# Optimization experiments

Hardware: AMD Instinct MI355X
Metric: run time of the kernel (lower is better)

Reference implementation:

```python
import math
import jax, jax.numpy as jnp
import numpy as np

B, FIN, FOUT, M = 8192, 512, 512, 8
INV_SQRT_2PI = 1.0 / math.sqrt(2.0 * math.pi)
SQRT_HALF = math.sqrt(0.5)


def setup_inputs() -> dict:
    key = jax.random.key(0)
    k = jax.random.split(key, 7)
    x = jax.random.normal(k[0], (B, FIN), dtype=jnp.float32)
    nan_mask = jax.random.uniform(k[1], (B, FIN)) < 0.15
    nan_mask = nan_mask.at[:, 0].set(True)  # every row has >=1 NaN -> GMM path taken, den > 0
    x = jnp.where(nan_mask, jnp.nan, x)
    bound = 1.0 / math.sqrt(FIN)  # torch nn.Linear default init range
    W = jax.random.uniform(k[2], (FOUT, FIN), dtype=jnp.float32, minval=-bound, maxval=bound)
    b = jax.random.uniform(k[3], (FOUT,), dtype=jnp.float32, minval=-bound, maxval=bound)
    mean_p = 0.1 * jax.random.normal(k[4], (M, FIN), dtype=jnp.float32)
    log_std2 = 0.1 * jax.random.normal(k[5], (M, FIN), dtype=jnp.float32)
    log_weights = jax.random.normal(k[6], (M,), dtype=jnp.float32)
    return {"x": x, "W": W, "b": b, "mean_p": mean_p,
            "log_std2": log_std2, "log_weights": log_weights}


def _nr(z):
    # pdf(z) + z * Phi(z), the Gaussian 'nr' function from the paper
    pdf = INV_SQRT_2PI * jnp.exp(-0.5 * z * z)
    return pdf + z * 0.5 * (1.0 + jax.lax.erf(z * SQRT_HALF))


def reference(x, W, b, mean_p, log_std2, log_weights):
    nan = jnp.isnan(x)                         # [B, FIN]
    empty = jnp.any(nan, axis=-1)[:, None]     # [B, 1]
    mask = nan[:, None, :]                     # [B, 1, FIN]
    # impute NaNs with per-mode GMM means
    mean = jnp.where(mask, mean_p, x[:, None, :])                   # [B, M, FIN]
    num = jnp.einsum('bmf,of->bom', mean, W) + b[None, :, None]     # [B, FOUT, M]
    std2 = jnp.where(mask, jnp.exp(log_std2), jnp.float32(0.0))     # [B, M, FIN]
    den = jnp.sqrt(jnp.einsum('bmf,of->bom', std2, W * W))          # [B, FOUT, M]
    nr = den * _nr(num / (den + 1e-9))                              # [B, FOUT, M]
    mixture = nr @ jax.nn.softmax(log_weights)                      # [B, FOUT]
    return jnp.where(empty, mixture, jax.nn.relu(num[..., 0]))
```

## Files before the change

kernel.cpp:

```cpp
#include <hip/hip_runtime.h>
#include <math.h>

typedef __attribute__((ext_vector_type(8))) short short8;
typedef __attribute__((ext_vector_type(8))) _Float16 f16x8;
typedef __attribute__((ext_vector_type(4))) float floatx4;
typedef __attribute__((ext_vector_type(4))) int intx4;
typedef __attribute__((ext_vector_type(16))) int intx16;

#define B_ROWS 8192
#define FIN    512
#define FOUT   512
#define QSN    4096.0f
#define QINVN  0.000244140625f
#define QSD    32768.0f
#define QINVD  0.000030517578125f

#define WSB_SW   0UL
#define WSB_CNT  64UL
#define WSB_BASE 65536UL
#define WSB_XCH  16842752UL
#define WSB_MSK  25231360UL
#define WSB_WH   33619968UL
#define WSB_BCT  34144256UL

__device__ __forceinline__ void gl2lds16(const void* g, void* l) {
    __builtin_amdgcn_global_load_lds((const __attribute__((address_space(1))) void*)g,
                                     (__attribute__((address_space(3))) void*)l,
                                     16, 0, 0);
}

__device__ __forceinline__ float frcp(float x) { float r; asm("v_rcp_f32 %0, %1" : "=v"(r) : "v"(x)); return r; }
__device__ __forceinline__ float frsq(float x) { float r; asm("v_rsq_f32 %0, %1" : "=v"(r) : "v"(x)); return r; }
__device__ __forceinline__ float fexp2(float x){ float r; asm("v_exp_f32 %0, %1" : "=v"(r) : "v"(x)); return r; }

__global__ __launch_bounds__(256) void prep_all(const float* __restrict__ W,
                                                const float* __restrict__ mean_p,
                                                const float* __restrict__ ls2,
                                                const float* __restrict__ x,
                                                const float* __restrict__ lw,
                                                signed char* __restrict__ bct,
                                                _Float16* __restrict__ Wh,
                                                _Float16* __restrict__ xch,
                                                signed char* __restrict__ msk,
                                                int* __restrict__ cnts,
                                                float* __restrict__ wsf) {
    int tid = threadIdx.x, lane = tid & 63, wid = tid >> 6;
    if (blockIdx.x < 2048) {
        int n  = blockIdx.x * 4 + wid;
        int fc = lane << 3;
        int o = n >> 4, t = n & 15;
        const float* wp = W + (size_t)o * FIN + fc;
        float v[8];
        float qs;
        if (t < 8) {
            const float* mp = mean_p + (size_t)t * FIN + fc;
#pragma unroll
            for (int j = 0; j < 8; ++j) v[j] = mp[j] * wp[j];
            qs = QSN;
            if (t == 0) {
                f16x8 wv;
#pragma unroll
                for (int j = 0; j < 8; ++j) wv[j] = (_Float16)wp[j];
                *(f16x8*)(Wh + (size_t)o * FIN + fc) = wv;
            }
        } else {
            const float* lp = ls2 + (size_t)(t - 8) * FIN + fc;
#pragma unroll
            for (int j = 0; j < 8; ++j) v[j] = fexp2(lp[j] * 1.4426950408889634f) * wp[j] * wp[j];
            qs = QSD;
        }
        unsigned long long pack = 0;
#pragma unroll
        for (int j = 0; j < 8; ++j) {
            int q = (int)rintf(v[j] * qs);
            q = q > 127 ? 127 : (q < -127 ? -127 : q);
            pack |= ((unsigned long long)(unsigned char)(signed char)q) << (8 * j);
        }
        *(unsigned long long*)(bct + (size_t)n * FIN + fc) = pack;
    } else {
        int row = (blockIdx.x - 2048) * 4 + wid;
        const float* xr = x + (size_t)row * FIN + lane * 8;
        float4 a = *(const float4*)xr;
        float4 b = *(const float4*)(xr + 4);
        float v[8] = {a.x, a.y, a.z, a.w, b.x, b.y, b.z, b.w};
        f16x8 xo;
        unsigned long long mpack = 0;
        bool anyn = false;
#pragma unroll
        for (int j = 0; j < 8; ++j) {
            bool isn = (v[j] != v[j]);
            anyn |= isn;
            xo[j] = (_Float16)(isn ? 0.f : v[j]);
            mpack |= ((unsigned long long)(isn ? 1u : 0u)) << (8 * j);
        }
        *(f16x8*)(xch + (size_t)row * FIN + lane * 8) = xo;
        *(unsigned long long*)(msk + (size_t)row * FIN + lane * 8) = mpack;
        bool any = __any(anyn);
        if (lane == 0) cnts[row] = any ? 1 : 0;
        if (blockIdx.x == 2048 && tid == 0) {
            float mx = lw[0];
            for (int m = 1; m < 8; ++m) mx = fmaxf(mx, lw[m]);
            float e[8]; float s = 0.f;
            for (int m = 0; m < 8; ++m) { e[m] = expf(lw[m] - mx); s += e[m]; }
            for (int m = 0; m < 8; ++m) wsf[m] = e[m] / s;
        }
    }
}

__global__ __launch_bounds__(256, 2) void gemm_base(const _Float16* __restrict__ xch,
                                                    const _Float16* __restrict__ Wh,
                                                    _Float16* __restrict__ base) {
    __shared__ char lds[73728];
    int tid = threadIdx.x, lane = tid & 63, wid = tid >> 6;
    int wr = wid >> 1, wc = wid & 1;
    int bb0 = blockIdx.y * 128;
    int ob0 = blockIdx.x * 64;

    const char* xB = (const char*)xch;
    const char* wB = (const char*)Wh;

    int rA0 = (wid +  0) * 8 + (lane >> 3);
    int rA1 = (wid +  4) * 8 + (lane >> 3);
    int rA2 = (wid +  8) * 8 + (lane >> 3);
    int rA3 = (wid + 12) * 8 + (lane >> 3);
    const char* gA0 = xB + (size_t)(bb0 + rA0) * 1024 + (((lane & 7) ^ (rA0 & 7)) << 4);
    const char* gA1 = xB + (size_t)(bb0 + rA1) * 1024 + (((lane & 7) ^ (rA1 & 7)) << 4);
    const char* gA2 = xB + (size_t)(bb0 + rA2) * 1024 + (((lane & 7) ^ (rA2 & 7)) << 4);
    const char* gA3 = xB + (size_t)(bb0 + rA3) * 1024 + (((lane & 7) ^ (rA3 & 7)) << 4);
    const char* gB0 = wB + (size_t)(ob0 + rA0) * 1024 + (((lane & 7) ^ (rA0 & 7)) << 4);
    const char* gB1 = wB + (size_t)(ob0 + rA1) * 1024 + (((lane & 7) ^ (rA1 & 7)) << 4);
    const int lA0o = (wid +  0) * 1024, lA1o = (wid +  4) * 1024;
    const int lA2o = (wid +  8) * 1024, lA3o = (wid + 12) * 1024;
    const int lB0o = 16384 + (wid + 0) * 1024, lB1o = 16384 + (wid + 4) * 1024;

    int offA[4], offB[2];
#pragma unroll
    for (int mi = 0; mi < 4; ++mi) {
        int r = wr * 64 + mi * 16 + (lane & 15);
        offA[mi] = r * 128 + ((((lane >> 4) ^ (r & 7))) << 4);
    }
#pragma unroll
    for (int ni = 0; ni < 2; ++ni) {
        int r = wc * 32 + ni * 16 + (lane & 15);
        offB[ni] = 16384 + r * 128 + ((((lane >> 4) ^ (r & 7))) << 4);
    }

    floatx4 acc[4][2];
#pragma unroll
    for (int mi = 0; mi < 4; ++mi)
#pragma unroll
        for (int ni = 0; ni < 2; ++ni) acc[mi][ni] = (floatx4){0.f, 0.f, 0.f, 0.f};

#define STAGEB(T)                                            \
    {                                                        \
        const int bo_ = ((T) % 3) * 24576;                   \
        gl2lds16(gA0 + (T) * 128, lds + bo_ + lA0o);         \
        gl2lds16(gA1 + (T) * 128, lds + bo_ + lA1o);         \
        gl2lds16(gA2 + (T) * 128, lds + bo_ + lA2o);         \
        gl2lds16(gA3 + (T) * 128, lds + bo_ + lA3o);         \
        gl2lds16(gB0 + (T) * 128, lds + bo_ + lB0o);         \
        gl2lds16(gB1 + (T) * 128, lds + bo_ + lB1o);         \
    }

    STAGEB(0); STAGEB(1);

#pragma unroll
    for (int t = 0; t < 8; ++t) {
        if (t < 7) asm volatile("s_waitcnt vmcnt(6)" ::: "memory");
        else       asm volatile("s_waitcnt vmcnt(0)" ::: "memory");
        __builtin_amdgcn_s_barrier();
        asm volatile("" ::: "memory");
        if (t + 2 < 8) STAGEB(t + 2);

        const int bo = (t % 3) * 24576;
#pragma unroll
        for (int kk = 0; kk < 2; ++kk) {
            const int kx = kk << 6;
            f16x8 av[4], bv[2];
#pragma unroll
            for (int mi = 0; mi < 4; ++mi) av[mi] = *(const f16x8*)(lds + bo + (offA[mi] ^ kx));
#pragma unroll
            for (int ni = 0; ni < 2; ++ni) bv[ni] = *(const f16x8*)(lds + bo + (offB[ni] ^ kx));
            __builtin_amdgcn_s_setprio(1);
#pragma unroll
            for (int mi = 0; mi < 4; ++mi)
#pragma unroll
                for (int ni = 0; ni < 2; ++ni)
                    acc[mi][ni] = __builtin_amdgcn_mfma_f32_16x16x32_f16(av[mi], bv[ni], acc[mi][ni], 0, 0, 0);
            __builtin_amdgcn_s_setprio(0);
        }
    }
#undef STAGEB

#pragma unroll
    for (int mi = 0; mi < 4; ++mi)
#pragma unroll
        for (int ni = 0; ni < 2; ++ni)
#pragma unroll
            for (int r = 0; r < 4; ++r) {
                int row = bb0 + wr * 64 + mi * 16 + (lane >> 4) * 4 + r;
                int col = ob0 + wc * 32 + ni * 16 + (lane & 15);
                base[((size_t)row << 9) + col] = (_Float16)acc[mi][ni][r];
            }
}

__global__ __launch_bounds__(256, 2) void gmm_fused(const signed char* __restrict__ msk,
                                                    const signed char* __restrict__ bct,
                                                    const float* __restrict__ wsf,
                                                    const int* __restrict__ cnts,
                                                    const _Float16* __restrict__ baseh,
                                                    const float* __restrict__ bias,
                                                    float* __restrict__ out) {
    __shared__ char lds[73728];

    int tid = threadIdx.x, lane = tid & 63, wid = tid >> 6;
    int wr = wid >> 1, wc = wid & 1;

    int id = blockIdx.x, g = id >> 8, wi = id & 255;
    int my = (g >> 2) * 16 + (wi >> 4);
    int nx = (g & 3) * 16 + (wi & 15);
    int b0 = my * 256, n0 = nx * 128;

    const char* mB = (const char*)msk;
    const char* bB = (const char*)bct;

    int cl = lane & 31, oh = lane >> 5;
    _Float16 base_r[4][2];
    float bias_r[2];
    int cnt_r[4];
#pragma unroll
    for (int ni = 0; ni < 2; ++ni) bias_r[ni] = bias[nx * 8 + wc * 4 + ni * 2 + oh];
#pragma unroll
    for (int mi = 0; mi < 4; ++mi) {
        int b = b0 + wr * 128 + mi * 32 + cl;
        cnt_r[mi] = cnts[b];
#pragma unroll
        for (int ni = 0; ni < 2; ++ni)
            base_r[mi][ni] = baseh[((size_t)b << 9) + nx * 8 + wc * 4 + ni * 2 + oh];
    }

    int rA0 = (wid +  0) * 16 + (lane >> 2);
    int rA1 = (wid +  4) * 16 + (lane >> 2);
    int rA2 = (wid +  8) * 16 + (lane >> 2);
    int rA3 = (wid + 12) * 16 + (lane >> 2);
    const char* gA0 = mB + (size_t)(b0 + rA0) * 512 + (((lane & 3) ^ ((rA0 >> 1) & 3)) << 4);
    const char* gA1 = mB + (size_t)(b0 + rA1) * 512 + (((lane & 3) ^ ((rA1 >> 1) & 3)) << 4);
    const char* gA2 = mB + (size_t)(b0 + rA2) * 512 + (((lane & 3) ^ ((rA2 >> 1) & 3)) << 4);
    const char* gA3 = mB + (size_t)(b0 + rA3) * 512 + (((lane & 3) ^ ((rA3 >> 1) & 3)) << 4);
    const char* gB0 = bB + (size_t)(n0 + rA0) * 512 + (((lane & 3) ^ ((rA0 >> 1) & 3)) << 4);
    const char* gB1 = bB + (size_t)(n0 + rA1) * 512 + (((lane & 3) ^ ((rA1 >> 1) & 3)) << 4);
    const int lA0o = (wid +  0) * 1024, lA1o = (wid +  4) * 1024;
    const int lA2o = (wid +  8) * 1024, lA3o = (wid + 12) * 1024;
    const int lB0o = 16384 + (wid + 0) * 1024, lB1o = 16384 + (wid + 4) * 1024;

    int offA[4], offB[2];
#pragma unroll
    for (int mi = 0; mi < 4; ++mi) {
        int r = wr * 128 + mi * 32 + (lane & 31);
        offA[mi] = r * 64 + ((((lane >> 5) ^ ((r >> 1) & 3))) << 4);
    }
#pragma unroll
    for (int ni = 0; ni < 2; ++ni) {
        int r = wc * 64 + ni * 32 + (lane & 31);
        offB[ni] = 16384 + r * 64 + ((((lane >> 5) ^ ((r >> 1) & 3))) << 4);
    }

    intx16 acc[4][2];
#pragma unroll
    for (int mi = 0; mi < 4; ++mi)
#pragma unroll
        for (int ni = 0; ni < 2; ++ni)
#pragma unroll
            for (int e = 0; e < 16; ++e) acc[mi][ni][e] = 0;

#define STAGE(T)                                             \
    {                                                        \
        const int bo_ = ((T) % 3) * 24576;                   \
        gl2lds16(gA0 + (T) * 64, lds + bo_ + lA0o);          \
        gl2lds16(gA1 + (T) * 64, lds + bo_ + lA1o);          \
        gl2lds16(gA2 + (T) * 64, lds + bo_ + lA2o);          \
        gl2lds16(gA3 + (T) * 64, lds + bo_ + lA3o);          \
        gl2lds16(gB0 + (T) * 64, lds + bo_ + lB0o);          \
        gl2lds16(gB1 + (T) * 64, lds + bo_ + lB1o);          \
    }

    STAGE(0); STAGE(1);

#pragma unroll
    for (int t = 0; t < 8; ++t) {
        if (t < 7) asm volatile("s_waitcnt vmcnt(6)" ::: "memory");
        else       asm volatile("s_waitcnt vmcnt(0)" ::: "memory");
        __builtin_amdgcn_s_barrier();
        asm volatile("" ::: "memory");
        if (t + 2 < 8) STAGE(t + 2);

        const int bo = (t % 3) * 24576;
#pragma unroll
        for (int kk = 0; kk < 2; ++kk) {
            const int kx = kk << 5;
            intx4 av[4], bv[2];
#pragma unroll
            for (int mi = 0; mi < 4; ++mi) av[mi] = *(const intx4*)(lds + bo + (offA[mi] ^ kx));
#pragma unroll
            for (int ni = 0; ni < 2; ++ni) bv[ni] = *(const intx4*)(lds + bo + (offB[ni] ^ kx));
            __builtin_amdgcn_s_setprio(1);
#pragma unroll
            for (int mi = 0; mi < 4; ++mi)
#pragma unroll
                for (int ni = 0; ni < 2; ++ni)
                    acc[mi][ni] = __builtin_amdgcn_mfma_i32_32x32x32_i8(av[mi], bv[ni], acc[mi][ni], 0, 0, 0);
            __builtin_amdgcn_s_setprio(0);
        }
    }
#undef STAGE

    __syncthreads();

    float swv[8];
#pragma unroll
    for (int m = 0; m < 8; ++m) swv[m] = wsf[m];

    int* sci = (int*)lds + wid * 1056;

#pragma unroll
    for (int mi = 0; mi < 4; ++mi) {
#pragma unroll
        for (int ni = 0; ni < 2; ++ni) {
#pragma unroll
            for (int reg = 0; reg < 16; ++reg) {
                int r = (reg & 3) + 8 * (reg >> 2) + 4 * oh;
                sci[r * 33 + cl] = acc[mi][ni][reg];
            }
            __asm__ volatile("s_waitcnt lgkmcnt(0)" ::: "memory");

            float cn[8], cd[8];
#pragma unroll
            for (int tt = 0; tt < 8; ++tt) cn[tt] = (float)sci[cl * 33 + oh * 16 + tt] * QINVN;
#pragma unroll
            for (int tt = 0; tt < 8; ++tt) cd[tt] = (float)sci[cl * 33 + oh * 16 + 8 + tt] * QINVD;

            int b = b0 + wr * 128 + mi * 32 + cl;
            int o = nx * 8 + wc * 4 + ni * 2 + oh;
            float K0 = (float)base_r[mi][ni] + bias_r[ni];
            bool empty = cnt_r[mi] > 0;

            float mix = 0.f, num0 = 0.f;
#pragma unroll
            for (int m = 0; m < 8; ++m) {
                float num = K0 + cn[m];
                if (m == 0) num0 = num;
                float rs  = frsq(fmaxf(cd[m], 1e-20f));
                float den = cd[m] * rs;
                float z   = num * rs;
                float az  = fabsf(z);
                float E   = fexp2((z * z) * -0.72134752044448170f);
                float t1  = frcp(fmaf(0.2316419f, az, 1.0f));
                float h   = fmaf(t1, 0.5307027145f, -0.7265760135f);
                h = fmaf(t1, h, 0.7107068705f);
                h = fmaf(t1, h, -0.142248368f);
                h = fmaf(t1, h, 0.127414796f);
                float u   = t1 * h;
                float v   = fmaf(-az, u, 0.3989422804014327f);
                float gg  = fmaf(E, v, fmaxf(z, 0.f));
                mix = fmaf(swv[m], den * gg, mix);
            }
            out[((size_t)b << 9) + o] = empty ? mix : fmaxf(num0, 0.f);
        }
    }
}

extern "C" void kernel_launch(void* const* d_in, const int* in_sizes, int n_in,
                              void* d_out, int out_size, void* d_ws, size_t ws_size,
                              hipStream_t stream) {
    const float* x        = (const float*)d_in[0];
    const float* W        = (const float*)d_in[1];
    const float* bvec     = (const float*)d_in[2];
    const float* mean_p   = (const float*)d_in[3];
    const float* log_std2 = (const float*)d_in[4];
    const float* lw       = (const float*)d_in[5];
    float* out = (float*)d_out;

    char* wsb = (char*)d_ws;
    float*        wsf  = (float*)wsb;
    int*          cnts = (int*)(wsb + WSB_CNT);
    _Float16*     base = (_Float16*)(wsb + WSB_BASE);
    _Float16*     xch  = (_Float16*)(wsb + WSB_XCH);
    signed char*  msk  = (signed char*)(wsb + WSB_MSK);
    _Float16*     Wh   = (_Float16*)(wsb + WSB_WH);
    signed char*  bct  = (signed char*)(wsb + WSB_BCT);

    prep_all<<<4096, 256, 0, stream>>>(W, mean_p, log_std2, x, lw, bct, Wh, xch, msk, cnts, wsf);
    gemm_base<<<dim3(FOUT / 64, B_ROWS / 128), 256, 0, stream>>>(xch, Wh, base);
    gmm_fused<<<(B_ROWS / 256) * (8192 / 128), 256, 0, stream>>>(msk, bct, wsf, cnts, base, bvec, out);
}
```

Baseline: 83.57 us.

## Use 8-wave blocks with smaller per-wave tiles and XCD-aware block mapping

The gmm_fused kernel now runs 512 threads per block. Each wave computes a 64x64 output tile instead of 128x64, so the int8 MFMA accumulators and A-fragment loads are halved, and staging is split across 8 waves with fewer async loads per wave. Block-to-tile mapping is also reorganised so consecutive block IDs on the same XCD share row tiles, which should improve L2 reuse. The launch bound asks for 4 blocks of 512 threads, which may cap VGPRs tightly enough to cause spills, and LDS use per block likely still limits residency anyway.

```diff
diff --git a/kernel.cpp b/kernel.cpp
--- a/kernel.cpp
+++ b/kernel.cpp
@@ -204,7 +204,7 @@
             }
 }
 
-__global__ __launch_bounds__(256, 2) void gmm_fused(const signed char* __restrict__ msk,
+__global__ __launch_bounds__(512, 4) void gmm_fused(const signed char* __restrict__ msk,
                                                     const signed char* __restrict__ bct,
                                                     const float* __restrict__ wsf,
                                                     const int* __restrict__ cnts,
@@ -216,47 +216,44 @@
     int tid = threadIdx.x, lane = tid & 63, wid = tid >> 6;
     int wr = wid >> 1, wc = wid & 1;
 
-    int id = blockIdx.x, g = id >> 8, wi = id & 255;
-    int my = (g >> 2) * 16 + (wi >> 4);
-    int nx = (g & 3) * 16 + (wi & 15);
+    int id = blockIdx.x;
+    int xcd = id & 7, pos = id >> 3;
+    int my = xcd * 4 + (pos & 3);
+    int nx = pos >> 2;
     int b0 = my * 256, n0 = nx * 128;
 
     const char* mB = (const char*)msk;
     const char* bB = (const char*)bct;
 
     int cl = lane & 31, oh = lane >> 5;
-    _Float16 base_r[4][2];
+    _Float16 base_r[2][2];
     float bias_r[2];
-    int cnt_r[4];
-#pragma unroll
-    for (int ni = 0; ni < 2; ++ni) bias_r[ni] = bias[nx * 8 + wc * 4 + ni * 2 + oh];
-#pragma unroll
-    for (int mi = 0; mi < 4; ++mi) {
-        int b = b0 + wr * 128 + mi * 32 + cl;
+    int cnt_r[2];
+#pragma unroll
+    for (int ni = 0; ni < 2; ++ni) bias_r[ni] = bias[(n0 >> 4) + wc * 4 + ni * 2 + oh];
+#pragma unroll
+    for (int mi = 0; mi < 2; ++mi) {
+        int b = b0 + wr * 64 + mi * 32 + cl;
         cnt_r[mi] = cnts[b];
 #pragma unroll
         for (int ni = 0; ni < 2; ++ni)
-            base_r[mi][ni] = baseh[((size_t)b << 9) + nx * 8 + wc * 4 + ni * 2 + oh];
-    }
-
-    int rA0 = (wid +  0) * 16 + (lane >> 2);
-    int rA1 = (wid +  4) * 16 + (lane >> 2);
-    int rA2 = (wid +  8) * 16 + (lane >> 2);
-    int rA3 = (wid + 12) * 16 + (lane >> 2);
+            base_r[mi][ni] = baseh[((size_t)b << 9) + (n0 >> 4) + wc * 4 + ni * 2 + oh];
+    }
+
+    int rA0 = (wid + 0) * 16 + (lane >> 2);
+    int rA1 = (wid + 8) * 16 + (lane >> 2);
+    int rB0 = rA0;
     const char* gA0 = mB + (size_t)(b0 + rA0) * 512 + (((lane & 3) ^ ((rA0 >> 1) & 3)) << 4);
     const char* gA1 = mB + (size_t)(b0 + rA1) * 512 + (((lane & 3) ^ ((rA1 >> 1) & 3)) << 4);
-    const char* gA2 = mB + (size_t)(b0 + rA2) * 512 + (((lane & 3) ^ ((rA2 >> 1) & 3)) << 4);
-    const char* gA3 = mB + (size_t)(b0 + rA3) * 512 + (((lane & 3) ^ ((rA3 >> 1) & 3)) << 4);
-    const char* gB0 = bB + (size_t)(n0 + rA0) * 512 + (((lane & 3) ^ ((rA0 >> 1) & 3)) << 4);
-    const char* gB1 = bB + (size_t)(n0 + rA1) * 512 + (((lane & 3) ^ ((rA1 >> 1) & 3)) << 4);
-    const int lA0o = (wid +  0) * 1024, lA1o = (wid +  4) * 1024;
-    const int lA2o = (wid +  8) * 1024, lA3o = (wid + 12) * 1024;
-    const int lB0o = 16384 + (wid + 0) * 1024, lB1o = 16384 + (wid + 4) * 1024;
-
-    int offA[4], offB[2];
-#pragma unroll
-    for (int mi = 0; mi < 4; ++mi) {
-        int r = wr * 128 + mi * 32 + (lane & 31);
+    const char* gB0 = bB + (size_t)(n0 + rB0) * 512 + (((lane & 3) ^ ((rB0 >> 1) & 3)) << 4);
+    const int lA0o = (wid + 0) * 1024;
+    const int lA1o = (wid + 8) * 1024;
+    const int lB0o = 16384 + wid * 1024;
+
+    int offA[2], offB[2];
+#pragma unroll
+    for (int mi = 0; mi < 2; ++mi) {
+        int r = wr * 64 + mi * 32 + (lane & 31);
         offA[mi] = r * 64 + ((((lane >> 5) ^ ((r >> 1) & 3))) << 4);
     }
 #pragma unroll
@@ -265,9 +262,9 @@
         offB[ni] = 16384 + r * 64 + ((((lane >> 5) ^ ((r >> 1) & 3))) << 4);
     }
 
-    intx16 acc[4][2];
-#pragma unroll
-    for (int mi = 0; mi < 4; ++mi)
+    intx16 acc[2][2];
+#pragma unroll
+    for (int mi = 0; mi < 2; ++mi)
 #pragma unroll
         for (int ni = 0; ni < 2; ++ni)
 #pragma unroll
@@ -278,17 +275,14 @@
         const int bo_ = ((T) % 3) * 24576;                   \
         gl2lds16(gA0 + (T) * 64, lds + bo_ + lA0o);          \
         gl2lds16(gA1 + (T) * 64, lds + bo_ + lA1o);          \
-        gl2lds16(gA2 + (T) * 64, lds + bo_ + lA2o);          \
-        gl2lds16(gA3 + (T) * 64, lds + bo_ + lA3o);          \
         gl2lds16(gB0 + (T) * 64, lds + bo_ + lB0o);          \
-        gl2lds16(gB1 + (T) * 64, lds + bo_ + lB1o);          \
     }
 
     STAGE(0); STAGE(1);
 
 #pragma unroll
     for (int t = 0; t < 8; ++t) {
-        if (t < 7) asm volatile("s_waitcnt vmcnt(6)" ::: "memory");
+        if (t < 7) asm volatile("s_waitcnt vmcnt(3)" ::: "memory");
         else       asm volatile("s_waitcnt vmcnt(0)" ::: "memory");
         __builtin_amdgcn_s_barrier();
         asm volatile("" ::: "memory");
@@ -298,14 +292,14 @@
 #pragma unroll
         for (int kk = 0; kk < 2; ++kk) {
             const int kx = kk << 5;
-            intx4 av[4], bv[2];
-#pragma unroll
-            for (int mi = 0; mi < 4; ++mi) av[mi] = *(const intx4*)(lds + bo + (offA[mi] ^ kx));
+            intx4 av[2], bv[2];
+#pragma unroll
+            for (int mi = 0; mi < 2; ++mi) av[mi] = *(const intx4*)(lds + bo + (offA[mi] ^ kx));
 #pragma unroll
             for (int ni = 0; ni < 2; ++ni) bv[ni] = *(const intx4*)(lds + bo + (offB[ni] ^ kx));
             __builtin_amdgcn_s_setprio(1);
 #pragma unroll
-            for (int mi = 0; mi < 4; ++mi)
+            for (int mi = 0; mi < 2; ++mi)
 #pragma unroll
                 for (int ni = 0; ni < 2; ++ni)
                     acc[mi][ni] = __builtin_amdgcn_mfma_i32_32x32x32_i8(av[mi], bv[ni], acc[mi][ni], 0, 0, 0);
@@ -323,7 +317,7 @@
     int* sci = (int*)lds + wid * 1056;
 
 #pragma unroll
-    for (int mi = 0; mi < 4; ++mi) {
+    for (int mi = 0; mi < 2; ++mi) {
 #pragma unroll
         for (int ni = 0; ni < 2; ++ni) {
 #pragma unroll
@@ -339,8 +333,8 @@
 #pragma unroll
             for (int tt = 0; tt < 8; ++tt) cd[tt] = (float)sci[cl * 33 + oh * 16 + 8 + tt] * QINVD;
 
-            int b = b0 + wr * 128 + mi * 32 + cl;
-            int o = nx * 8 + wc * 4 + ni * 2 + oh;
+            int b = b0 + wr * 64 + mi * 32 + cl;
+            int o = (n0 >> 4) + wc * 4 + ni * 2 + oh;
             float K0 = (float)base_r[mi][ni] + bias_r[ni];
             bool empty = cnt_r[mi] > 0;
 
@@ -391,5 +385,5 @@
 
     prep_all<<<4096, 256, 0, stream>>>(W, mean_p, log_std2, x, lw, bct, Wh, xch, msk, cnts, wsf);
     gemm_base<<<dim3(FOUT / 64, B_ROWS / 128), 256, 0, stream>>>(xch, Wh, base);
-    gmm_fused<<<(B_ROWS / 256) * (8192 / 128), 256, 0, stream>>>(msk, bct, wsf, cnts, base, bvec, out);
-}
+    gmm_fused<<<(B_ROWS / 256) * (8192 / 128), 512, 0, stream>>>(msk, bct, wsf, cnts, base, bvec, out);
+}
```

After: 77.57 us. -7.2%, faster.
